# Optimization experiments

Measured on AMD Instinct MI355X. Metric: run time of the kernel, lower is better.

Reference implementation:

```python
import jax, jax.numpy as jnp
import numpy as np

IN_C, HID, L, NN, BS, OUT = 32, 128, 4, 64, 512, 3
N = NN * BS  # total graph vertices
EPS_LN = 1e-5
EPS_SM = 1e-16  # PyG softmax eps


def setup_inputs() -> dict:
    key = jax.random.key(0)
    ks = jax.random.split(key, 16)
    E = 524288
    x = jax.random.normal(ks[0], (N, IN_C), dtype=jnp.float32)
    edge_index = jax.random.randint(ks[1], (2, E), 0, N, dtype=jnp.int64)
    s = 0.1
    # first GAT layer (in -> hidden)
    W0 = jax.random.normal(ks[2], (IN_C, HID), dtype=jnp.float32) * s
    att_src0 = jax.random.normal(ks[3], (HID,), dtype=jnp.float32) * s
    att_dst0 = jax.random.normal(ks[4], (HID,), dtype=jnp.float32) * s
    bias0 = jnp.zeros((HID,), dtype=jnp.float32)
    # residual GAT layers (hidden -> hidden), stacked over L
    W_res = jax.random.normal(ks[5], (L, HID, HID), dtype=jnp.float32) * s
    att_src_res = jax.random.normal(ks[6], (L, HID), dtype=jnp.float32) * s
    att_dst_res = jax.random.normal(ks[7], (L, HID), dtype=jnp.float32) * s
    bias_res = jnp.zeros((L, HID), dtype=jnp.float32)
    gamma = jnp.ones((L, HID), dtype=jnp.float32)
    beta = jnp.zeros((L, HID), dtype=jnp.float32)
    # per-node predictor heads
    W1p = jax.random.normal(ks[8], (NN, HID, HID // 2), dtype=jnp.float32) * s
    W2p = jax.random.normal(ks[9], (NN, HID // 2, OUT), dtype=jnp.float32) * s
    return {"x": x, "edge_index": edge_index, "W0": W0, "att_src0": att_src0,
            "att_dst0": att_dst0, "bias0": bias0, "W_res": W_res,
            "att_src_res": att_src_res, "att_dst_res": att_dst_res,
            "bias_res": bias_res, "gamma": gamma, "beta": beta,
            "W1p": W1p, "W2p": W2p}


def _gat(x, src, dst, W, a_src, a_dst, b):
    # PyG GATConv, heads=1, negative_slope=0.2, self-loops already appended
    h = x @ W                                   # [N, H]
    a_s = (h * a_src).sum(-1)                   # [N]
    a_d = (h * a_dst).sum(-1)                   # [N]
    e = jax.nn.leaky_relu(a_s[src] + a_d[dst], 0.2)   # [E]
    m = jax.ops.segment_max(e, dst, num_segments=N)
    e = jnp.exp(e - m[dst])
    z = jax.ops.segment_sum(e, dst, num_segments=N)
    alpha = e / (z[dst] + EPS_SM)               # [E]
    out = jax.ops.segment_sum(h[src] * alpha[:, None], dst, num_segments=N)
    return out + b


def _layernorm(x, g, b):
    mu = x.mean(-1, keepdims=True)
    var = ((x - mu) ** 2).mean(-1, keepdims=True)
    return (x - mu) * jax.lax.rsqrt(var + EPS_LN) * g + b


def reference(x, edge_index, W0, att_src0, att_dst0, bias0, W_res,
              att_src_res, att_dst_res, bias_res, gamma, beta, W1p, W2p):
    loops = jnp.arange(N, dtype=edge_index.dtype)
    src = jnp.concatenate([edge_index[0], loops])
    dst = jnp.concatenate([edge_index[1], loops])
    # first GAT + relu
    h = jax.nn.relu(_gat(x, src, dst, W0, att_src0, att_dst0, bias0))
    # res+ blocks: h = h + conv(dropout(act(norm(h))))  (dropout=identity, eval)
    for i in range(L):
        t = jax.nn.relu(_layernorm(h, gamma[i], beta[i]))
        t = _gat(t, src, dst, W_res[i], att_src_res[i], att_dst_res[i], bias_res[i])
        h = h + t
    h = jax.nn.relu(_layernorm(h, gamma[0], beta[0]))
    # per-node predictor heads
    h = h.reshape(NN, BS, HID)
    t = jax.nn.relu(jnp.einsum('nbh,nhk->nbk', h, W1p))
    logits = jnp.einsum('nbk,nko->nbo', t, W2p)
    return jax.nn.softmax(logits, axis=-1)   # softmax over class dim (dim=1 per node slice)
```

## Files before the change

### kernel.cpp

```cpp
#include <hip/hip_runtime.h>
#include <hip/hip_fp8.h>
#include <math.h>

#define NND   32768
#define HIDD  128
#define NHEAD 64
#define BSS   512
#define OUTC  3
#define NTILES (NND / 16)
#define CSLOT 80

typedef _Float16 half_t;
typedef __attribute__((ext_vector_type(8))) _Float16 half8;
typedef __attribute__((ext_vector_type(4))) float f32x4;

__device__ __forceinline__ unsigned enc_fp8x4(float a, float b, float c, float d) {
    __hip_fp8x4_e4m3 q(make_float4(a, b, c, d));
    return (unsigned)q.__x;
}
__device__ __forceinline__ float4 dec_fp8x4(unsigned v) {
    __hip_fp8x4_e4m3 t; t.__x = (__hip_fp8x4_storage_t)v;
    return (float4)t;
}

// ... 43 lines not shown
                int tt = task - 64; int l = 1 + tt / 256; int r = tt % 256;
                int k = r >> 1; sd = r & 1;
                row = W_res + (size_t)(l - 1) * 16384 + k * 128;
                att = (sd ? ad_res : as_res) + (l - 1) * 128;
                slot = l * 128 + k;
            }
            float s = 0.f;
            for (int n = 0; n < 128; ++n) s += row[n] * att[n];
            (sd ? wvec + 640 : wvec)[slot] = s;
        }
    } else if (b < 1090) {
        int b2 = b - 578;
        const float* xs = x + (size_t)b2 * 64 * 32;
        half_t* xd = xh + (size_t)b2 * 64 * 32;
        for (int i = tid; i < 1024; i += 256) {
            float2 v = ((const float2*)xs)[i];
            union { unsigned u; half_t h[2]; } cv;
            cv.h[0] = (half_t)v.x; cv.h[1] = (half_t)v.y;
            ((unsigned*)xd)[i] = cv.u;
        }
    } else {
        int j = (b - 1090) * 256 + tid;
        int Etot = E + NND;
        if (j >= Etot) return;
        int src, dst;
        if (j < E) { src = ei[j]; dst = ei[E + j]; }
        else       { src = j - E; dst = j - E; }
        int rank = atomicAdd(&counts[dst], 1);
        if (rank < CSLOT) csrd[(size_t)dst * CSLOT + rank] = src;
    }
}

__global__ __launch_bounds__(256) void a0_kernel(const half_t* __restrict__ xh,
        const float* __restrict__ wvec,
        float* __restrict__ a_s, float* __restrict__ a_d) {
    int tid = threadIdx.x;
    __shared__ float ws0[32], wd0[32];
    if (tid < 32) { ws0[tid] = wvec[tid]; wd0[tid] = wvec[640 + tid]; }
    __syncthreads();
    int g = blockIdx.x * 256 + tid;
    int node = g >> 2, part = g & 3;
    half8 xv = *(const half8*)&xh[(size_t)node * 32 + part * 8];
    float s = 0.f, d2 = 0.f;
#pragma unroll
    for (int j = 0; j < 8; ++j) { float f = (float)xv[j]; s += f * ws0[part * 8 + j]; d2 += f * wd0[part * 8 + j]; }
    s += __shfl_xor(s, 1); s += __shfl_xor(s, 2);
    d2 += __shfl_xor(d2, 1); d2 += __shfl_xor(d2, 2);
    if (part == 0) { a_s[node] = s; a_d[node] = d2; }
}


struct MArgs {
    const half_t* xh;
    const int* csrd;
    const int* counts;
    const half_t* W0t;
    const half_t* Wh;
    const float* bias0;
    const float* b_res;
    const float* gamma;
    const float* beta;
    const float* wvec;
    float* a_s0; float* a_d0; float* a_s1; float* a_d1;
    unsigned char* Th8a; unsigned char* Th8b;
    half_t* Hh;
    const half_t* W1h;
    const float* W2p;
    float* out;
};

struct SmemT {
    half_t Pt[16][136];
    union U {
        float vv[16][132];
        struct { int s[1024]; float p[1024]; } sp;
    } u;
    int cntl[16];
    float adv[16];
};

__device__ __forceinline__ void stage_sp(const float* __restrict__ a_sv,
        const int* __restrict__ csrd, int n0, int base, int tid, SmemT& sm) {
#pragma unroll
    for (int it = 0; it < 4; ++it) {
        int i = it * 256 + tid;
        int ln = i >> 6, k = i & 63;
        int sN = 0; float pN = 0.f;
        if (base + k < sm.cntl[ln]) {
            sN = csrd[(size_t)(n0 + ln) * CSLOT + base + k];
            float tt = a_sv[sN] + sm.adv[ln];
            tt = (tt > 0.f) ? tt : 0.2f * tt;
            pN = __expf(tt);
        }
        sm.u.sp.s[i] = sN;
        sm.u.sp.p[i] = pN;
    }
}

__device__ __forceinline__ void agg_node_f8(const unsigned char* __restrict__ F8,
        const SmemT& sm, int ln, int base, int lane, int q, int r15,
        float acc[8], float& pzv) {
    int rem = sm.cntl[ln] - base;
    if (rem <= 0) return;
    int cnt = rem > 64 ? 64 : rem;
    pzv += sm.u.sp.p[ln * 64 + lane];
    const int* sl = &sm.u.sp.s[ln * 64];
    const float* pl = &sm.u.sp.p[ln * 64];
    for (int k4 = 0; k4 < cnt; k4 += 16) {
        int s0 = sl[k4 + q],       s1 = sl[k4 + 4 + q];
        int s2 = sl[k4 + 8 + q],   s3 = sl[k4 + 12 + q];
        float p0 = pl[k4 + q],     p1 = pl[k4 + 4 + q];
        float p2 = pl[k4 + 8 + q], p3 = pl[k4 + 12 + q];
        uint2 r0 = *(const uint2*)&F8[(size_t)s0 * HIDD + r15 * 8];
        uint2 r1 = *(const uint2*)&F8[(size_t)s1 * HIDD + r15 * 8];
        uint2 r2 = *(const uint2*)&F8[(size_t)s2 * HIDD + r15 * 8];
        uint2 r3 = *(const uint2*)&F8[(size_t)s3 * HIDD + r15 * 8];
        float4 f;
        f = dec_fp8x4(r0.x); acc[0]+=p0*f.x; acc[1]+=p0*f.y; acc[2]+=p0*f.z; acc[3]+=p0*f.w;
        f = dec_fp8x4(r0.y); acc[4]+=p0*f.x; acc[5]+=p0*f.y; acc[6]+=p0*f.z; acc[7]+=p0*f.w;
        f = dec_fp8x4(r1.x); acc[0]+=p1*f.x; acc[1]+=p1*f.y; acc[2]+=p1*f.z; acc[3]+=p1*f.w;
        f = dec_fp8x4(r1.y); acc[4]+=p1*f.x; acc[5]+=p1*f.y; acc[6]+=p1*f.z; acc[7]+=p1*f.w;
        f = dec_fp8x4(r2.x); acc[0]+=p2*f.x; acc[1]+=p2*f.y; acc[2]+=p2*f.z; acc[3]+=p2*f.w;
        f = dec_fp8x4(r2.y); acc[4]+=p2*f.x; acc[5]+=p2*f.y; acc[6]+=p2*f.z; acc[7]+=p2*f.w;
        f = dec_fp8x4(r3.x); acc[0]+=p3*f.x; acc[1]+=p3*f.y; acc[2]+=p3*f.z; acc[3]+=p3*f.w;
        f = dec_fp8x4(r3.y); acc[4]+=p3*f.x; acc[5]+=p3*f.y; acc[6]+=p3*f.z; acc[7]+=p3*f.w;
    }
}

__device__ __forceinline__ void finish_res(SmemT& sm, int wv, int pass, int q, int r15,
        float acc[2][8], float pz2[2]) {
#pragma unroll
    for (int ln2 = 0; ln2 < 2; ++ln2) {
        int ln = wv * 4 + pass * 2 + ln2;
        float z = pz2[ln2];
#pragma unroll
        for (int o = 32; o; o >>= 1) z += __shfl_xor(z, o);
#pragma unroll
        for (int i = 0; i < 8; ++i) {
            acc[ln2][i] += __shfl_xor(acc[ln2][i], 16);
            acc[ln2][i] += __shfl_xor(acc[ln2][i], 32);
        }
        if (q == 0) {
            float inv = 1.f / (z + 1e-16f);
            union { int4 v; half_t hh[8]; } u;
#pragma unroll
            for (int i = 0; i < 8; ++i) u.hh[i] = (half_t)(acc[ln2][i] * inv);
            *(int4*)&sm.Pt[ln][r15 * 8] = u.v;
        }
    }
}

__device__ __forceinline__ void agg2_res(const unsigned char* __restrict__ F8,
        const float* __restrict__ a_sv, const float* __restrict__ a_dv,
        const int* __restrict__ csrd, const int* __restrict__ counts,
        int n0, int tid, int wv, int lane, int q, int r15, SmemT& sm) {
    if (tid < 16) { sm.cntl[tid] = counts[n0 + tid]; sm.adv[tid] = a_dv[n0 + tid]; }
    __syncthreads();
    int maxd = 0;
    for (int i = 0; i < 16; ++i) { int d = sm.cntl[i]; maxd = d > maxd ? d : maxd; }
    if (maxd <= 64) {
        stage_sp(a_sv, csrd, n0, 0, tid, sm);
        __syncthreads();
#pragma unroll
        for (int pass = 0; pass < 2; ++pass) {
            float acc[2][8];
            float pz2[2] = {0.f, 0.f};
#pragma unroll
            for (int a = 0; a < 2; ++a)
#pragma unroll
                for (int i = 0; i < 8; ++i) acc[a][i] = 0.f;
#pragma unroll
            for (int ln2 = 0; ln2 < 2; ++ln2)
                agg_node_f8(F8, sm, wv * 4 + pass * 2 + ln2, 0, lane, q, r15, acc[ln2], pz2[ln2]);
            finish_res(sm, wv, pass, q, r15, acc, pz2);
        }
    } else {
#pragma unroll
        for (int pass = 0; pass < 2; ++pass) {
            float acc[2][8];
            float pz2[2] = {0.f, 0.f};
#pragma unroll
            for (int a = 0; a < 2; ++a)
#pragma unroll
                for (int i = 0; i < 8; ++i) acc[a][i] = 0.f;
            for (int base = 0; base < maxd; base += 64) {
                __syncthreads();
                stage_sp(a_sv, csrd, n0, base, tid, sm);
                __syncthreads();
#pragma unroll
                for (int ln2 = 0; ln2 < 2; ++ln2)
                    agg_node_f8(F8, sm, wv * 4 + pass * 2 + ln2, base, lane, q, r15, acc[ln2], pz2[ln2]);
            }
            finish_res(sm, wv, pass, q, r15, acc, pz2);
        }
    }
}

__device__ __forceinline__ void agg2_l0(const half_t* __restrict__ xh,
        const float* __restrict__ a_sv, const float* __restrict__ a_dv,
        const int* __restrict__ csrd, const int* __restrict__ counts,
        int n0, int tid, int wv, int lane, int q, int r15, SmemT& sm) {
    if (tid < 16) { sm.cntl[tid] = counts[n0 + tid]; sm.adv[tid] = a_dv[n0 + tid]; }
    __syncthreads();
    int maxd = 0;
    for (int i = 0; i < 16; ++i) { int d = sm.cntl[i]; maxd = d > maxd ? d : maxd; }
    float acc[4][2];
    float pz[4];
#pragma unroll
    for (int a = 0; a < 4; ++a) { pz[a] = 0.f; acc[a][0] = 0.f; acc[a][1] = 0.f; }
    for (int base = 0; base < maxd; base += 64) {
        __syncthreads();
        stage_sp(a_sv, csrd, n0, base, tid, sm);
        __syncthreads();
#pragma unroll
        for (int ln4 = 0; ln4 < 4; ++ln4) {
            int ln = wv * 4 + ln4;
            int rem = sm.cntl[ln] - base;
            if (rem <= 0) continue;
            int cnt = rem > 64 ? 64 : rem;
            pz[ln4] += sm.u.sp.p[ln * 64 + lane];
            const int* sl = &sm.u.sp.s[ln * 64];
            const float* pl = &sm.u.sp.p[ln * 64];
            for (int k4 = 0; k4 < cnt; k4 += 16) {
                int s0 = sl[k4 + q],      s1 = sl[k4 + 4 + q];
                int s2 = sl[k4 + 8 + q],  s3 = sl[k4 + 12 + q];
                float p0 = pl[k4 + q],    p1 = pl[k4 + 4 + q];
                float p2 = pl[k4 + 8 + q], p3 = pl[k4 + 12 + q];
                union { unsigned u; half_t h[2]; } u0, u1, u2, u3;
                u0.u = *(const unsigned*)&xh[(size_t)s0 * 32 + r15 * 2];
                u1.u = *(const unsigned*)&xh[(size_t)s1 * 32 + r15 * 2];
                u2.u = *(const unsigned*)&xh[(size_t)s2 * 32 + r15 * 2];
                u3.u = *(const unsigned*)&xh[(size_t)s3 * 32 + r15 * 2];
                acc[ln4][0] += p0 * (float)u0.h[0] + p1 * (float)u1.h[0] + p2 * (float)u2.h[0] + p3 * (float)u3.h[0];
                acc[ln4][1] += p0 * (float)u0.h[1] + p1 * (float)u1.h[1] + p2 * (float)u2.h[1] + p3 * (float)u3.h[1];
            }
        }
    }
#pragma unroll
    for (int ln4 = 0; ln4 < 4; ++ln4) {
        int ln = wv * 4 + ln4;
        float z = pz[ln4];
#pragma unroll
        for (int o = 32; o; o >>= 1) z += __shfl_xor(z, o);
#pragma unroll
        for (int i = 0; i < 2; ++i) {
            acc[ln4][i] += __shfl_xor(acc[ln4][i], 16);
            acc[ln4][i] += __shfl_xor(acc[ln4][i], 32);
        }
        if (q == 0) {
            float inv = 1.f / (z + 1e-16f);
            union { unsigned u; half_t h[2]; } w2;
            w2.h[0] = (half_t)(acc[ln4][0] * inv);
            w2.h[1] = (half_t)(acc[ln4][1] * inv);
            *(unsigned*)&sm.Pt[ln][r15 * 2] = w2.u;
        }
    }
}

template <int K, bool RES>
__device__ __forceinline__ void gemm_epi_tile(int n0, int tid, int wv, int q, int r15,
        const half_t* __restrict__ Whl, const float* __restrict__ bias,
        half_t* __restrict__ Hh, unsigned char* __restrict__ Th8o,
        const float* __restrict__ gamma, const float* __restrict__ beta,
        const float* __restrict__ wsn, const float* __restrict__ wdn,
        float* __restrict__ as_out, float* __restrict__ ad_out,
        half_t Pt[16][136], float vv[16][132]) {
    half8 afrag[K / 32];
#pragma unroll
    for (int s = 0; s < K / 32; ++s)
        afrag[s] = *(const half8*)&Pt[r15][s * 32 + q * 8];
    f32x4 acc2[2];
#pragma unroll
    for (int i = 0; i < 2; ++i) {
        int ct = wv * 2 + i;
        f32x4 c = {0.f, 0.f, 0.f, 0.f};
#pragma unroll
        for (int s = 0; s < K / 32; ++s) {
            half8 bfrag = *(const half8*)&Whl[(size_t)(ct * 16 + r15) * K + s * 32 + q * 8];
            c = __builtin_amdgcn_mfma_f32_16x16x32_f16(afrag[s], bfrag, c, 0, 0, 0);
        }
        acc2[i] = c;
    }
#pragma unroll
    for (int i = 0; i < 2; ++i)
#pragma unroll
        for (int r = 0; r < 4; ++r)
            vv[q * 4 + r][wv * 32 + i * 16 + r15] = acc2[i][r];
    __syncthreads();
    int grp = tid >> 4, sub = tid & 15;
    int node = n0 + grp;
    const float* vrow = &vv[grp][sub * 8];
    float v8[8];
    {
        float4 bi0 = *(const float4*)&bias[sub * 8];
        float4 bi1 = *(const float4*)&bias[sub * 8 + 4];
        v8[0] = vrow[0] + bi0.x; v8[1] = vrow[1] + bi0.y;
        v8[2] = vrow[2] + bi0.z; v8[3] = vrow[3] + bi0.w;
        v8[4] = vrow[4] + bi1.x; v8[5] = vrow[5] + bi1.y;
        v8[6] = vrow[6] + bi1.z; v8[7] = vrow[7] + bi1.w;
    }
    if (RES) {
        half8 hold = *(const half8*)&Hh[(size_t)node * HIDD + sub * 8];
#pragma unroll
        for (int j = 0; j < 8; ++j) v8[j] += (float)hold[j];
    } else {
#pragma unroll
        for (int j = 0; j < 8; ++j) v8[j] = fmaxf(v8[j], 0.f);
    }
    union { int4 i4; half_t h[8]; } hw;
#pragma unroll
    for (int j = 0; j < 8; ++j) hw.h[j] = (half_t)v8[j];
    *(int4*)&Hh[(size_t)node * HIDD + sub * 8] = hw.i4;
    float sum = 0.f;
#pragma unroll
    for (int j = 0; j < 8; ++j) sum += v8[j];
#pragma unroll
    for (int o = 8; o; o >>= 1) sum += __shfl_xor(sum, o);
    float mu = sum * (1.f / HIDD);
    float var = 0.f;
#pragma unroll
    for (int j = 0; j < 8; ++j) { float dx = v8[j] - mu; var += dx * dx; }
#pragma unroll
    for (int o = 8; o; o >>= 1) var += __shfl_xor(var, o);
    float rs = rsqrtf(var * (1.f / HIDD) + 1e-5f);
    float asn, adn;
    uint2 tw;
    {
        float4 g4 = *(const float4*)&gamma[sub * 8];
        float4 b4 = *(const float4*)&beta[sub * 8];
        float t0 = fmaxf((v8[0] - mu) * rs * g4.x + b4.x, 0.f);
        float t1 = fmaxf((v8[1] - mu) * rs * g4.y + b4.y, 0.f);
        float t2 = fmaxf((v8[2] - mu) * rs * g4.z + b4.z, 0.f);
        float t3 = fmaxf((v8[3] - mu) * rs * g4.w + b4.w, 0.f);
        float4 w4 = *(const float4*)&wsn[sub * 8];
        float4 d4 = *(const float4*)&wdn[sub * 8];
        asn = t0 * w4.x; asn += t1 * w4.y; asn += t2 * w4.z; asn += t3 * w4.w;
        adn = t0 * d4.x; adn += t1 * d4.y; adn += t2 * d4.z; adn += t3 * d4.w;
        tw.x = enc_fp8x4(t0, t1, t2, t3);
    }
    {
        float4 g4 = *(const float4*)&gamma[sub * 8 + 4];
        float4 b4 = *(const float4*)&beta[sub * 8 + 4];
        float t4 = fmaxf((v8[4] - mu) * rs * g4.x + b4.x, 0.f);
        float t5 = fmaxf((v8[5] - mu) * rs * g4.y + b4.y, 0.f);
        float t6 = fmaxf((v8[6] - mu) * rs * g4.z + b4.z, 0.f);
        float t7 = fmaxf((v8[7] - mu) * rs * g4.w + b4.w, 0.f);
        float4 w4 = *(const float4*)&wsn[sub * 8 + 4];
        float4 d4 = *(const float4*)&wdn[sub * 8 + 4];
        asn += t4 * w4.x; asn += t5 * w4.y; asn += t6 * w4.z; asn += t7 * w4.w;
        adn += t4 * d4.x; adn += t5 * d4.y; adn += t6 * d4.z; adn += t7 * d4.w;
        tw.y = enc_fp8x4(t4, t5, t6, t7);
    }
    *(uint2*)&Th8o[(size_t)node * HIDD + sub * 8] = tw;
#pragma unroll
    for (int o = 8; o; o >>= 1) { asn += __shfl_xor(asn, o); adn += __shfl_xor(adn, o); }
    if (sub == 0) { as_out[node] = asn; ad_out[node] = adn; }
}

__device__ __forceinline__ void last_tile(int n0, int tid, int wv, int q, int r15,
        const MArgs& A, half_t Pt[16][136], float vv[16][132]) {
    const half_t* Whl = A.Wh + (size_t)3 * 16384;
    half8 afrag[4];
#pragma unroll
    for (int s = 0; s < 4; ++s)
        afrag[s] = *(const half8*)&Pt[r15][s * 32 + q * 8];
    f32x4 acc2[2];
#pragma unroll
    for (int i = 0; i < 2; ++i) {
        int ct = wv * 2 + i;
        f32x4 c = {0.f, 0.f, 0.f, 0.f};
#pragma unroll
        for (int s = 0; s < 4; ++s) {
            half8 bfrag = *(const half8*)&Whl[(size_t)(ct * 16 + r15) * 128 + s * 32 + q * 8];
            c = __builtin_amdgcn_mfma_f32_16x16x32_f16(afrag[s], bfrag, c, 0, 0, 0);
        }
        acc2[i] = c;
    }
#pragma unroll
    for (int i = 0; i < 2; ++i)
#pragma unroll
        for (int r = 0; r < 4; ++r)
            vv[q * 4 + r][wv * 32 + i * 16 + r15] = acc2[i][r];
    __syncthreads();
    int grp = tid >> 4, sub = tid & 15;
    const float* bias = A.b_res + 3 * HIDD;
    float4 bi0 = *(const float4*)&bias[sub * 8],    bi1 = *(const float4*)&bias[sub * 8 + 4];
    float4 g0  = *(const float4*)&A.gamma[sub * 8], g1  = *(const float4*)&A.gamma[sub * 8 + 4];
    float4 be0 = *(const float4*)&A.beta[sub * 8],  be1 = *(const float4*)&A.beta[sub * 8 + 4];
    float bi[8] = {bi0.x,bi0.y,bi0.z,bi0.w,bi1.x,bi1.y,bi1.z,bi1.w};
    float gg[8] = {g0.x,g0.y,g0.z,g0.w,g1.x,g1.y,g1.z,g1.w};
    float be[8] = {be0.x,be0.y,be0.z,be0.w,be1.x,be1.y,be1.z,be1.w};
    int node = n0 + grp;
    float v8[8];
    half8 hold = *(const half8*)&A.Hh[(size_t)node * HIDD + sub * 8];
#pragma unroll
    for (int j = 0; j < 8; ++j) v8[j] = vv[grp][sub * 8 + j] + bi[j] + (float)hold[j];
    float sum = 0.f;
#pragma unroll
    for (int j = 0; j < 8; ++j) sum += v8[j];
#pragma unroll
    for (int o = 8; o; o >>= 1) sum += __shfl_xor(sum, o);
    float mu = sum * (1.f / HIDD);
    float var = 0.f;
#pragma unroll
    for (int j = 0; j < 8; ++j) { float dx = v8[j] - mu; var += dx * dx; }
#pragma unroll
    for (int o = 8; o; o >>= 1) var += __shfl_xor(var, o);
    float rs = rsqrtf(var * (1.f / HIDD) + 1e-5f);
    union { int4 i4; half_t h[8]; } u;
#pragma unroll
    for (int j = 0; j < 8; ++j)
        u.h[j] = (half_t)fmaxf((v8[j] - mu) * rs * gg[j] + be[j], 0.f);
    __syncthreads();
    *(int4*)&Pt[grp][sub * 8] = u.i4;
    __syncthreads();
    int head = n0 >> 9;
    const half_t* W1g = A.W1h + (size_t)head * 64 * 128;
    half8 pa[4];
#pragma unroll
    for (int s = 0; s < 4; ++s)
        pa[s] = *(const half8*)&Pt[r15][s * 32 + q * 8];
    int n2 = wv * 16 + r15;
    f32x4 c = {0.f, 0.f, 0.f, 0.f};
#pragma unroll
    for (int s = 0; s < 4; ++s) {
        half8 bfrag = *(const half8*)&W1g[(size_t)n2 * 128 + s * 32 + q * 8];
        c = __builtin_amdgcn_mfma_f32_16x16x32_f16(pa[s], bfrag, c, 0, 0, 0);
    }
    float w2a = A.W2p[(size_t)head * 192 + n2 * 3 + 0];
    float w2b = A.W2p[(size_t)head * 192 + n2 * 3 + 1];
    float w2c = A.W2p[(size_t)head * 192 + n2 * 3 + 2];
    float lg[3][4];
#pragma unroll
    for (int r = 0; r < 4; ++r) {
        float t = fmaxf(c[r], 0.f);
        lg[0][r] = t * w2a;
        lg[1][r] = t * w2b;
        lg[2][r] = t * w2c;
    }
#pragma unroll
    for (int o = 8; o; o >>= 1)
#pragma unroll
        for (int oo = 0; oo < 3; ++oo)
#pragma unroll
            for (int r = 0; r < 4; ++r) lg[oo][r] += __shfl_xor(lg[oo][r], o);
    __syncthreads();
    if (r15 == 0) {
#pragma unroll
        for (int r = 0; r < 4; ++r)
#pragma unroll
            for (int oo = 0; oo < 3; ++oo) vv[q * 4 + r][wv * 3 + oo] = lg[oo][r];
    }
    __syncthreads();
    if (tid < 16) {
        float l0 = vv[tid][0] + vv[tid][3] + vv[tid][6] + vv[tid][9];
        float l1 = vv[tid][1] + vv[tid][4] + vv[tid][7] + vv[tid][10];
        float l2 = vv[tid][2] + vv[tid][5] + vv[tid][8] + vv[tid][11];
        float mx = fmaxf(l0, fmaxf(l1, l2));
        float e0 = __expf(l0 - mx), e1 = __expf(l1 - mx), e2 = __expf(l2 - mx);
        float inv = 1.f / (e0 + e1 + e2);
        float* op = A.out + (size_t)(n0 + tid) * OUTC;
        op[0] = e0 * inv; op[1] = e1 * inv; op[2] = e2 * inv;
    }
}

__global__ __launch_bounds__(256, 8) void fused6_l0(MArgs A) {
    __shared__ SmemT sm;
    int tid = threadIdx.x;
    int wv = tid >> 6, lane = tid & 63;
    int q = lane >> 4, r15 = lane & 15;
    int n0 = blockIdx.x * 16;
    agg2_l0(A.xh, A.a_s0, A.a_d0, A.csrd, A.counts, n0, tid, wv, lane, q, r15, sm);
    __syncthreads();
    gemm_epi_tile<32, false>(n0, tid, wv, q, r15, A.W0t, A.bias0, A.Hh, A.Th8a,
        A.gamma, A.beta, A.wvec + 128, A.wvec + 640 + 128, A.a_s1, A.a_d1, sm.Pt, sm.u.vv);
}

template <int L>
__global__ __launch_bounds__(256, 8) void fused6_res(MArgs A) {
    __shared__ SmemT sm;
    int tid = threadIdx.x;
    int wv = tid >> 6, lane = tid & 63;
    int q = lane >> 4, r15 = lane & 15;
    int n0 = blockIdx.x * 16;
    const unsigned char* Ts = (L & 1) ? A.Th8b : A.Th8a;
    unsigned char* Td       = (L & 1) ? A.Th8a : A.Th8b;
    const float* asv = (L & 1) ? A.a_s0 : A.a_s1;
    const float* adv = (L & 1) ? A.a_d0 : A.a_d1;
    float* aso = (L & 1) ? A.a_s1 : A.a_s0;
    float* ado = (L & 1) ? A.a_d1 : A.a_d0;
    agg2_res(Ts, asv, adv, A.csrd, A.counts, n0, tid, wv, lane, q, r15, sm);
    __syncthreads();
    gemm_epi_tile<128, true>(n0, tid, wv, q, r15, A.Wh + (size_t)L * 16384,
        A.b_res + L * HIDD, A.Hh, Td, A.gamma + (L + 1) * HIDD, A.beta + (L + 1) * HIDD,
        A.wvec + (L + 2) * 128, A.wvec + 640 + (L + 2) * 128, aso, ado, sm.Pt, sm.u.vv);
}

__global__ __launch_bounds__(256, 4) void fused6_last(MArgs A) {
    __shared__ SmemT sm;
    int tid = threadIdx.x;
    int wv = tid >> 6, lane = tid & 63;
    int q = lane >> 4, r15 = lane & 15;
    int n0 = blockIdx.x * 16;
    agg2_res(A.Th8b, A.a_s0, A.a_d0, A.csrd, A.counts, n0, tid, wv, lane, q, r15, sm);
    __syncthreads();
    last_tile(n0, tid, wv, q, r15, A, sm.Pt, sm.u.vv);
}

extern "C" void kernel_launch(void* const* d_in, const int* in_sizes, int n_in,
                              void* d_out, int out_size, void* d_ws, size_t ws_size,
                              hipStream_t stream) {
    const float* x        = (const float*)d_in[0];
    const int*   ei       = (const int*)d_in[1];
    const float* W0       = (const float*)d_in[2];
    const float* att_src0 = (const float*)d_in[3];
    const float* att_dst0 = (const float*)d_in[4];
    const float* bias0    = (const float*)d_in[5];
    const float* W_res    = (const float*)d_in[6];
    const float* as_res   = (const float*)d_in[7];
    const float* ad_res   = (const float*)d_in[8];
    const float* b_res    = (const float*)d_in[9];
    const float* gamma    = (const float*)d_in[10];
    const float* beta     = (const float*)d_in[11];
    const float* W1p      = (const float*)d_in[12];
    const float* W2p      = (const float*)d_in[13];
    float* out = (float*)d_out;

    int E = in_sizes[1] / 2;
    int Etot = E + NND;

    char* p = (char*)d_ws;
    auto alloc = [&](size_t bytes) { void* r = (void*)p; p += (bytes + 255) & ~(size_t)255; return r; };
    int*    counts  = (int*)alloc((size_t)NND * 4);
    int*    csrd    = (int*)alloc((size_t)NND * CSLOT * 4);
    half_t* xh      = (half_t*)alloc((size_t)NND * 32 * 2);
    unsigned char* Th8a = (unsigned char*)alloc((size_t)NND * HIDD);
    unsigned char* Th8b = (unsigned char*)alloc((size_t)NND * HIDD);
    half_t* Hh      = (half_t*)alloc((size_t)NND * HIDD * 2);
    float*  a_s0    = (float*)alloc((size_t)NND * 4);
    float*  a_d0    = (float*)alloc((size_t)NND * 4);
    float*  a_s1    = (float*)alloc((size_t)NND * 4);
    float*  a_d1    = (float*)alloc((size_t)NND * 4);
    half_t* Wh      = (half_t*)alloc((size_t)4 * HIDD * HIDD * 2);
    half_t* W1h     = (half_t*)alloc((size_t)NHEAD * 64 * HIDD * 2);
    half_t* W0t     = (half_t*)alloc((size_t)HIDD * 32 * 2);
    float*  wvec    = (float*)alloc((size_t)1280 * 4);

    int egrid = (Etot + 255) / 256;

    hipMemsetAsync(counts, 0, (size_t)NND * 4, stream);
    prep_kernel<<<1090 + egrid, 256, 0, stream>>>(W0, W_res, W1p, att_src0, att_dst0,
        as_res, ad_res, x, ei, E, Wh, W1h, W0t, wvec, xh, counts, csrd);
    a0_kernel<<<512, 256, 0, stream>>>(xh, wvec, a_s0, a_d0);

    MArgs ma;
    ma.xh = xh; ma.csrd = csrd; ma.counts = counts;
    ma.W0t = W0t; ma.Wh = Wh;
    ma.bias0 = bias0; ma.b_res = b_res;
    ma.gamma = gamma; ma.beta = beta; ma.wvec = wvec;
    ma.a_s0 = a_s0; ma.a_d0 = a_d0; ma.a_s1 = a_s1; ma.a_d1 = a_d1;
    ma.Th8a = Th8a; ma.Th8b = Th8b; ma.Hh = Hh;
    ma.W1h = W1h; ma.W2p = W2p; ma.out = out;

    fused6_l0<<<NTILES, 256, 0, stream>>>(ma);
    fused6_res<0><<<NTILES, 256, 0, stream>>>(ma);
    fused6_res<1><<<NTILES, 256, 0, stream>>>(ma);
    fused6_res<2><<<NTILES, 256, 0, stream>>>(ma);
    fused6_last<<<NTILES, 256, 0, stream>>>(ma);
}
```

Before: 292.7 us.

## Double block size to 512 threads so each wave aggregates two nodes

```diff
diff --git a/kernel.cpp b/kernel.cpp
--- a/kernel.cpp
+++ b/kernel.cpp
@@ -149,8 +149,8 @@
 __device__ __forceinline__ void stage_sp(const float* __restrict__ a_sv,
         const int* __restrict__ csrd, int n0, int base, int tid, SmemT& sm) {
 #pragma unroll
-    for (int it = 0; it < 4; ++it) {
-        int i = it * 256 + tid;
+    for (int it = 0; it < 2; ++it) {
+        int i = it * 512 + tid;
         int ln = i >> 6, k = i & 63;
         int sN = 0; float pN = 0.f;
         if (base + k < sm.cntl[ln]) {
@@ -164,59 +164,6 @@
     }
 }
 
-__device__ __forceinline__ void agg_node_f8(const unsigned char* __restrict__ F8,
-        const SmemT& sm, int ln, int base, int lane, int q, int r15,
-        float acc[8], float& pzv) {
-    int rem = sm.cntl[ln] - base;
-    if (rem <= 0) return;
-    int cnt = rem > 64 ? 64 : rem;
-    pzv += sm.u.sp.p[ln * 64 + lane];
-    const int* sl = &sm.u.sp.s[ln * 64];
-    const float* pl = &sm.u.sp.p[ln * 64];
-    for (int k4 = 0; k4 < cnt; k4 += 16) {
-        int s0 = sl[k4 + q],       s1 = sl[k4 + 4 + q];
-        int s2 = sl[k4 + 8 + q],   s3 = sl[k4 + 12 + q];
-        float p0 = pl[k4 + q],     p1 = pl[k4 + 4 + q];
-        float p2 = pl[k4 + 8 + q], p3 = pl[k4 + 12 + q];
-        uint2 r0 = *(const uint2*)&F8[(size_t)s0 * HIDD + r15 * 8];
-        uint2 r1 = *(const uint2*)&F8[(size_t)s1 * HIDD + r15 * 8];
-        uint2 r2 = *(const uint2*)&F8[(size_t)s2 * HIDD + r15 * 8];
-        uint2 r3 = *(const uint2*)&F8[(size_t)s3 * HIDD + r15 * 8];
-        float4 f;
-        f = dec_fp8x4(r0.x); acc[0]+=p0*f.x; acc[1]+=p0*f.y; acc[2]+=p0*f.z; acc[3]+=p0*f.w;
-        f = dec_fp8x4(r0.y); acc[4]+=p0*f.x; acc[5]+=p0*f.y; acc[6]+=p0*f.z; acc[7]+=p0*f.w;
-        f = dec_fp8x4(r1.x); acc[0]+=p1*f.x; acc[1]+=p1*f.y; acc[2]+=p1*f.z; acc[3]+=p1*f.w;
-        f = dec_fp8x4(r1.y); acc[4]+=p1*f.x; acc[5]+=p1*f.y; acc[6]+=p1*f.z; acc[7]+=p1*f.w;
-        f = dec_fp8x4(r2.x); acc[0]+=p2*f.x; acc[1]+=p2*f.y; acc[2]+=p2*f.z; acc[3]+=p2*f.w;
-        f = dec_fp8x4(r2.y); acc[4]+=p2*f.x; acc[5]+=p2*f.y; acc[6]+=p2*f.z; acc[7]+=p2*f.w;
-        f = dec_fp8x4(r3.x); acc[0]+=p3*f.x; acc[1]+=p3*f.y; acc[2]+=p3*f.z; acc[3]+=p3*f.w;
-        f = dec_fp8x4(r3.y); acc[4]+=p3*f.x; acc[5]+=p3*f.y; acc[6]+=p3*f.z; acc[7]+=p3*f.w;
-    }
-}
-
-__device__ __forceinline__ void finish_res(SmemT& sm, int wv, int pass, int q, int r15,
-        float acc[2][8], float pz2[2]) {
-#pragma unroll
-    for (int ln2 = 0; ln2 < 2; ++ln2) {
-        int ln = wv * 4 + pass * 2 + ln2;
-        float z = pz2[ln2];
-#pragma unroll
-        for (int o = 32; o; o >>= 1) z += __shfl_xor(z, o);
-#pragma unroll
-        for (int i = 0; i < 8; ++i) {
-            acc[ln2][i] += __shfl_xor(acc[ln2][i], 16);
-            acc[ln2][i] += __shfl_xor(acc[ln2][i], 32);
-        }
-        if (q == 0) {
-            float inv = 1.f / (z + 1e-16f);
-            union { int4 v; half_t hh[8]; } u;
-#pragma unroll
-            for (int i = 0; i < 8; ++i) u.hh[i] = (half_t)(acc[ln2][i] * inv);
-            *(int4*)&sm.Pt[ln][r15 * 8] = u.v;
-        }
-    }
-}
-
 __device__ __forceinline__ void agg2_res(const unsigned char* __restrict__ F8,
         const float* __restrict__ a_sv, const float* __restrict__ a_dv,
         const int* __restrict__ csrd, const int* __restrict__ counts,
@@ -225,40 +172,74 @@
     __syncthreads();
     int maxd = 0;
     for (int i = 0; i < 16; ++i) { int d = sm.cntl[i]; maxd = d > maxd ? d : maxd; }
-    if (maxd <= 64) {
-        stage_sp(a_sv, csrd, n0, 0, tid, sm);
+    float acc[2][8];
+    float pz[2];
+#pragma unroll
+    for (int a = 0; a < 2; ++a) {
+        pz[a] = 0.f;
+#pragma unroll
+        for (int i = 0; i < 8; ++i) acc[a][i] = 0.f;
+    }
+    for (int base = 0; base < maxd; base += 64) {
         __syncthreads();
-#pragma unroll
-        for (int pass = 0; pass < 2; ++pass) {
-            float acc[2][8];
-            float pz2[2] = {0.f, 0.f};
-#pragma unroll
-            for (int a = 0; a < 2; ++a)
-#pragma unroll
-                for (int i = 0; i < 8; ++i) acc[a][i] = 0.f;
-#pragma unroll
-            for (int ln2 = 0; ln2 < 2; ++ln2)
-                agg_node_f8(F8, sm, wv * 4 + pass * 2 + ln2, 0, lane, q, r15, acc[ln2], pz2[ln2]);
-            finish_res(sm, wv, pass, q, r15, acc, pz2);
-        }
-    } else {
-#pragma unroll
-        for (int pass = 0; pass < 2; ++pass) {
-            float acc[2][8];
-            float pz2[2] = {0.f, 0.f};
-#pragma unroll
-            for (int a = 0; a < 2; ++a)
-#pragma unroll
-                for (int i = 0; i < 8; ++i) acc[a][i] = 0.f;
-            for (int base = 0; base < maxd; base += 64) {
-                __syncthreads();
-                stage_sp(a_sv, csrd, n0, base, tid, sm);
-                __syncthreads();
-#pragma unroll
-                for (int ln2 = 0; ln2 < 2; ++ln2)
-                    agg_node_f8(F8, sm, wv * 4 + pass * 2 + ln2, base, lane, q, r15, acc[ln2], pz2[ln2]);
+        stage_sp(a_sv, csrd, n0, base, tid, sm);
+        __syncthreads();
+#pragma unroll
+        for (int ln2 = 0; ln2 < 2; ++ln2) {
+            int ln = wv * 2 + ln2;
+            int rem = sm.cntl[ln] - base;
+            if (rem <= 0) continue;
+            int cnt = rem > 64 ? 64 : rem;
+            pz[ln2] += sm.u.sp.p[ln * 64 + lane];
+            const int* sl = &sm.u.sp.s[ln * 64];
+            const float* pl = &sm.u.sp.p[ln * 64];
+            int full = cnt & ~15;
+            int k4 = 0;
+            for (; k4 < full; k4 += 16) {
+                int s0 = sl[k4 + q],      s1 = sl[k4 + 4 + q];
+                int s2 = sl[k4 + 8 + q],  s3 = sl[k4 + 12 + q];
+                float p0 = pl[k4 + q],    p1 = pl[k4 + 4 + q];
+                float p2 = pl[k4 + 8 + q], p3 = pl[k4 + 12 + q];
+                uint2 r0 = *(const uint2*)&F8[(size_t)s0 * HIDD + r15 * 8];
+                uint2 r1 = *(const uint2*)&F8[(size_t)s1 * HIDD + r15 * 8];
+                uint2 r2 = *(const uint2*)&F8[(size_t)s2 * HIDD + r15 * 8];
+                uint2 r3 = *(const uint2*)&F8[(size_t)s3 * HIDD + r15 * 8];
+                float4 f;
+                f = dec_fp8x4(r0.x); acc[ln2][0]+=p0*f.x; acc[ln2][1]+=p0*f.y; acc[ln2][2]+=p0*f.z; acc[ln2][3]+=p0*f.w;
+                f = dec_fp8x4(r0.y); acc[ln2][4]+=p0*f.x; acc[ln2][5]+=p0*f.y; acc[ln2][6]+=p0*f.z; acc[ln2][7]+=p0*f.w;
+                f = dec_fp8x4(r1.x); acc[ln2][0]+=p1*f.x; acc[ln2][1]+=p1*f.y; acc[ln2][2]+=p1*f.z; acc[ln2][3]+=p1*f.w;
+                f = dec_fp8x4(r1.y); acc[ln2][4]+=p1*f.x; acc[ln2][5]+=p1*f.y; acc[ln2][6]+=p1*f.z; acc[ln2][7]+=p1*f.w;
+                f = dec_fp8x4(r2.x); acc[ln2][0]+=p2*f.x; acc[ln2][1]+=p2*f.y; acc[ln2][2]+=p2*f.z; acc[ln2][3]+=p2*f.w;
+                f = dec_fp8x4(r2.y); acc[ln2][4]+=p2*f.x; acc[ln2][5]+=p2*f.y; acc[ln2][6]+=p2*f.z; acc[ln2][7]+=p2*f.w;
+                f = dec_fp8x4(r3.x); acc[ln2][0]+=p3*f.x; acc[ln2][1]+=p3*f.y; acc[ln2][2]+=p3*f.z; acc[ln2][3]+=p3*f.w;
+                f = dec_fp8x4(r3.y); acc[ln2][4]+=p3*f.x; acc[ln2][5]+=p3*f.y; acc[ln2][6]+=p3*f.z; acc[ln2][7]+=p3*f.w;
             }
-            finish_res(sm, wv, pass, q, r15, acc, pz2);
+            for (; k4 < cnt; k4 += 4) {
+                int s0 = sl[k4 + q]; float p0 = pl[k4 + q];
+                uint2 r0 = *(const uint2*)&F8[(size_t)s0 * HIDD + r15 * 8];
+                float4 f;
+                f = dec_fp8x4(r0.x); acc[ln2][0]+=p0*f.x; acc[ln2][1]+=p0*f.y; acc[ln2][2]+=p0*f.z; acc[ln2][3]+=p0*f.w;
+                f = dec_fp8x4(r0.y); acc[ln2][4]+=p0*f.x; acc[ln2][5]+=p0*f.y; acc[ln2][6]+=p0*f.z; acc[ln2][7]+=p0*f.w;
+            }
+        }
+    }
+#pragma unroll
+    for (int ln2 = 0; ln2 < 2; ++ln2) {
+        int ln = wv * 2 + ln2;
+        float z = pz[ln2];
+#pragma unroll
+        for (int o = 32; o; o >>= 1) z += __shfl_xor(z, o);
+#pragma unroll
+        for (int i = 0; i < 8; ++i) {
+            acc[ln2][i] += __shfl_xor(acc[ln2][i], 16);
+            acc[ln2][i] += __shfl_xor(acc[ln2][i], 32);
+        }
+        if (q == 0) {
+            float inv = 1.f / (z + 1e-16f);
+            union { int4 v; half_t hh[8]; } u;
+#pragma unroll
+            for (int i = 0; i < 8; ++i) u.hh[i] = (half_t)(acc[ln2][i] * inv);
+            *(int4*)&sm.Pt[ln][r15 * 8] = u.v;
         }
     }
 }
@@ -271,24 +252,26 @@
     __syncthreads();
     int maxd = 0;
     for (int i = 0; i < 16; ++i) { int d = sm.cntl[i]; maxd = d > maxd ? d : maxd; }
-    float acc[4][2];
-    float pz[4];
-#pragma unroll
-    for (int a = 0; a < 4; ++a) { pz[a] = 0.f; acc[a][0] = 0.f; acc[a][1] = 0.f; }
+    float acc[2][2];
+    float pz[2];
+#pragma unroll
+    for (int a = 0; a < 2; ++a) { pz[a] = 0.f; acc[a][0] = 0.f; acc[a][1] = 0.f; }
     for (int base = 0; base < maxd; base += 64) {
         __syncthreads();
         stage_sp(a_sv, csrd, n0, base, tid, sm);
         __syncthreads();
 #pragma unroll
-        for (int ln4 = 0; ln4 < 4; ++ln4) {
-            int ln = wv * 4 + ln4;
+        for (int ln2 = 0; ln2 < 2; ++ln2) {
+            int ln = wv * 2 + ln2;
             int rem = sm.cntl[ln] - base;
             if (rem <= 0) continue;
             int cnt = rem > 64 ? 64 : rem;
-            pz[ln4] += sm.u.sp.p[ln * 64 + lane];
+            pz[ln2] += sm.u.sp.p[ln * 64 + lane];
             const int* sl = &sm.u.sp.s[ln * 64];
             const float* pl = &sm.u.sp.p[ln * 64];
-            for (int k4 = 0; k4 < cnt; k4 += 16) {
+            int full = cnt & ~15;
+            int k4 = 0;
+            for (; k4 < full; k4 += 16) {
                 int s0 = sl[k4 + q],      s1 = sl[k4 + 4 + q];
                 int s2 = sl[k4 + 8 + q],  s3 = sl[k4 + 12 + q];
                 float p0 = pl[k4 + q],    p1 = pl[k4 + 4 + q];
@@ -298,27 +281,34 @@
                 u1.u = *(const unsigned*)&xh[(size_t)s1 * 32 + r15 * 2];
                 u2.u = *(const unsigned*)&xh[(size_t)s2 * 32 + r15 * 2];
                 u3.u = *(const unsigned*)&xh[(size_t)s3 * 32 + r15 * 2];
-                acc[ln4][0] += p0 * (float)u0.h[0] + p1 * (float)u1.h[0] + p2 * (float)u2.h[0] + p3 * (float)u3.h[0];
-                acc[ln4][1] += p0 * (float)u0.h[1] + p1 * (float)u1.h[1] + p2 * (float)u2.h[1] + p3 * (float)u3.h[1];
+                acc[ln2][0] += p0 * (float)u0.h[0] + p1 * (float)u1.h[0] + p2 * (float)u2.h[0] + p3 * (float)u3.h[0];
+                acc[ln2][1] += p0 * (float)u0.h[1] + p1 * (float)u1.h[1] + p2 * (float)u2.h[1] + p3 * (float)u3.h[1];
             }
-        }
-    }
-#pragma unroll
-    for (int ln4 = 0; ln4 < 4; ++ln4) {
-        int ln = wv * 4 + ln4;
-        float z = pz[ln4];
+            for (; k4 < cnt; k4 += 4) {
+                int s0 = sl[k4 + q]; float p0 = pl[k4 + q];
+                union { unsigned u; half_t h[2]; } u0;
+                u0.u = *(const unsigned*)&xh[(size_t)s0 * 32 + r15 * 2];
+                acc[ln2][0] += p0 * (float)u0.h[0];
+                acc[ln2][1] += p0 * (float)u0.h[1];
+            }
+        }
+    }
+#pragma unroll
+    for (int ln2 = 0; ln2 < 2; ++ln2) {
+        int ln = wv * 2 + ln2;
+        float z = pz[ln2];
 #pragma unroll
         for (int o = 32; o; o >>= 1) z += __shfl_xor(z, o);
 #pragma unroll
         for (int i = 0; i < 2; ++i) {
-            acc[ln4][i] += __shfl_xor(acc[ln4][i], 16);
-            acc[ln4][i] += __shfl_xor(acc[ln4][i], 32);
+            acc[ln2][i] += __shfl_xor(acc[ln2][i], 16);
+            acc[ln2][i] += __shfl_xor(acc[ln2][i], 32);
         }
         if (q == 0) {
             float inv = 1.f / (z + 1e-16f);
             union { unsigned u; half_t h[2]; } w2;
-            w2.h[0] = (half_t)(acc[ln4][0] * inv);
-            w2.h[1] = (half_t)(acc[ln4][1] * inv);
+            w2.h[0] = (half_t)(acc[ln2][0] * inv);
+            w2.h[1] = (half_t)(acc[ln2][1] * inv);
             *(unsigned*)&sm.Pt[ln][r15 * 2] = w2.u;
         }
     }
@@ -336,92 +326,88 @@
 #pragma unroll
     for (int s = 0; s < K / 32; ++s)
         afrag[s] = *(const half8*)&Pt[r15][s * 32 + q * 8];
-    f32x4 acc2[2];
-#pragma unroll
-    for (int i = 0; i < 2; ++i) {
-        int ct = wv * 2 + i;
+    {
         f32x4 c = {0.f, 0.f, 0.f, 0.f};
 #pragma unroll
         for (int s = 0; s < K / 32; ++s) {
-            half8 bfrag = *(const half8*)&Whl[(size_t)(ct * 16 + r15) * K + s * 32 + q * 8];
+            half8 bfrag = *(const half8*)&Whl[(size_t)(wv * 16 + r15) * K + s * 32 + q * 8];
             c = __builtin_amdgcn_mfma_f32_16x16x32_f16(afrag[s], bfrag, c, 0, 0, 0);
         }
-        acc2[i] = c;
-    }
-#pragma unroll
-    for (int i = 0; i < 2; ++i)
 #pragma unroll
         for (int r = 0; r < 4; ++r)
-            vv[q * 4 + r][wv * 32 + i * 16 + r15] = acc2[i][r];
-    __syncthreads();
-    int grp = tid >> 4, sub = tid & 15;
-    int node = n0 + grp;
-    const float* vrow = &vv[grp][sub * 8];
-    float v8[8];
-    {
-        float4 bi0 = *(const float4*)&bias[sub * 8];
-        float4 bi1 = *(const float4*)&bias[sub * 8 + 4];
-        v8[0] = vrow[0] + bi0.x; v8[1] = vrow[1] + bi0.y;
-        v8[2] = vrow[2] + bi0.z; v8[3] = vrow[3] + bi0.w;
-        v8[4] = vrow[4] + bi1.x; v8[5] = vrow[5] + bi1.y;
-        v8[6] = vrow[6] + bi1.z; v8[7] = vrow[7] + bi1.w;
-    }
-    if (RES) {
-        half8 hold = *(const half8*)&Hh[(size_t)node * HIDD + sub * 8];
-#pragma unroll
-        for (int j = 0; j < 8; ++j) v8[j] += (float)hold[j];
-    } else {
-#pragma unroll
-        for (int j = 0; j < 8; ++j) v8[j] = fmaxf(v8[j], 0.f);
-    }
-    union { int4 i4; half_t h[8]; } hw;
-#pragma unroll
-    for (int j = 0; j < 8; ++j) hw.h[j] = (half_t)v8[j];
-    *(int4*)&Hh[(size_t)node * HIDD + sub * 8] = hw.i4;
-    float sum = 0.f;
-#pragma unroll
-    for (int j = 0; j < 8; ++j) sum += v8[j];
-#pragma unroll
-    for (int o = 8; o; o >>= 1) sum += __shfl_xor(sum, o);
-    float mu = sum * (1.f / HIDD);
-    float var = 0.f;
-#pragma unroll
-    for (int j = 0; j < 8; ++j) { float dx = v8[j] - mu; var += dx * dx; }
-#pragma unroll
-    for (int o = 8; o; o >>= 1) var += __shfl_xor(var, o);
-    float rs = rsqrtf(var * (1.f / HIDD) + 1e-5f);
-    float asn, adn;
-    uint2 tw;
-    {
-        float4 g4 = *(const float4*)&gamma[sub * 8];
-        float4 b4 = *(const float4*)&beta[sub * 8];
-        float t0 = fmaxf((v8[0] - mu) * rs * g4.x + b4.x, 0.f);
-        float t1 = fmaxf((v8[1] - mu) * rs * g4.y + b4.y, 0.f);
-        float t2 = fmaxf((v8[2] - mu) * rs * g4.z + b4.z, 0.f);
-        float t3 = fmaxf((v8[3] - mu) * rs * g4.w + b4.w, 0.f);
-        float4 w4 = *(const float4*)&wsn[sub * 8];
-        float4 d4 = *(const float4*)&wdn[sub * 8];
-        asn = t0 * w4.x; asn += t1 * w4.y; asn += t2 * w4.z; asn += t3 * w4.w;
-        adn = t0 * d4.x; adn += t1 * d4.y; adn += t2 * d4.z; adn += t3 * d4.w;
-        tw.x = enc_fp8x4(t0, t1, t2, t3);
-    }
-    {
-        float4 g4 = *(const float4*)&gamma[sub * 8 + 4];
-        float4 b4 = *(const float4*)&beta[sub * 8 + 4];
-        float t4 = fmaxf((v8[4] - mu) * rs * g4.x + b4.x, 0.f);
-        float t5 = fmaxf((v8[5] - mu) * rs * g4.y + b4.y, 0.f);
-        float t6 = fmaxf((v8[6] - mu) * rs * g4.z + b4.z, 0.f);
-        float t7 = fmaxf((v8[7] - mu) * rs * g4.w + b4.w, 0.f);
-        float4 w4 = *(const float4*)&wsn[sub * 8 + 4];
-        float4 d4 = *(const float4*)&wdn[sub * 8 + 4];
-        asn += t4 * w4.x; asn += t5 * w4.y; asn += t6 * w4.z; asn += t7 * w4.w;
-        adn += t4 * d4.x; adn += t5 * d4.y; adn += t6 * d4.z; adn += t7 * d4.w;
-        tw.y = enc_fp8x4(t4, t5, t6, t7);
-    }
-    *(uint2*)&Th8o[(size_t)node * HIDD + sub * 8] = tw;
-#pragma unroll
-    for (int o = 8; o; o >>= 1) { asn += __shfl_xor(asn, o); adn += __shfl_xor(adn, o); }
-    if (sub == 0) { as_out[node] = asn; ad_out[node] = adn; }
+            vv[q * 4 + r][wv * 16 + r15] = c[r];
+    }
+    __syncthreads();
+    if (tid < 256) {
+        int grp = tid >> 4, sub = tid & 15;
+        int node = n0 + grp;
+        const float* vrow = &vv[grp][sub * 8];
+        float v8[8];
+        {
+            float4 bi0 = *(const float4*)&bias[sub * 8];
+            float4 bi1 = *(const float4*)&bias[sub * 8 + 4];
+            v8[0] = vrow[0] + bi0.x; v8[1] = vrow[1] + bi0.y;
+            v8[2] = vrow[2] + bi0.z; v8[3] = vrow[3] + bi0.w;
+            v8[4] = vrow[4] + bi1.x; v8[5] = vrow[5] + bi1.y;
+            v8[6] = vrow[6] + bi1.z; v8[7] = vrow[7] + bi1.w;
+        }
+        if (RES) {
+            half8 hold = *(const half8*)&Hh[(size_t)node * HIDD + sub * 8];
+#pragma unroll
+            for (int j = 0; j < 8; ++j) v8[j] += (float)hold[j];
+        } else {
+#pragma unroll
+            for (int j = 0; j < 8; ++j) v8[j] = fmaxf(v8[j], 0.f);
+        }
+        union { int4 i4; half_t h[8]; } hw;
+#pragma unroll
+        for (int j = 0; j < 8; ++j) hw.h[j] = (half_t)v8[j];
+        *(int4*)&Hh[(size_t)node * HIDD + sub * 8] = hw.i4;
+        float sum = 0.f;
+#pragma unroll
+        for (int j = 0; j < 8; ++j) sum += v8[j];
+#pragma unroll
+        for (int o = 8; o; o >>= 1) sum += __shfl_xor(sum, o);
+        float mu = sum * (1.f / HIDD);
+        float var = 0.f;
+#pragma unroll
+        for (int j = 0; j < 8; ++j) { float dx = v8[j] - mu; var += dx * dx; }
+#pragma unroll
+        for (int o = 8; o; o >>= 1) var += __shfl_xor(var, o);
+        float rs = rsqrtf(var * (1.f / HIDD) + 1e-5f);
+        float asn, adn;
+        uint2 tw;
+        {
+            float4 g4 = *(const float4*)&gamma[sub * 8];
+            float4 b4 = *(const float4*)&beta[sub * 8];
+            float t0 = fmaxf((v8[0] - mu) * rs * g4.x + b4.x, 0.f);
+            float t1 = fmaxf((v8[1] - mu) * rs * g4.y + b4.y, 0.f);
+            float t2 = fmaxf((v8[2] - mu) * rs * g4.z + b4.z, 0.f);
+            float t3 = fmaxf((v8[3] - mu) * rs * g4.w + b4.w, 0.f);
+            float4 w4 = *(const float4*)&wsn[sub * 8];
+            float4 d4 = *(const float4*)&wdn[sub * 8];
+            asn = t0 * w4.x; asn += t1 * w4.y; asn += t2 * w4.z; asn += t3 * w4.w;
+            adn = t0 * d4.x; adn += t1 * d4.y; adn += t2 * d4.z; adn += t3 * d4.w;
+            tw.x = enc_fp8x4(t0, t1, t2, t3);
+        }
+        {
+            float4 g4 = *(const float4*)&gamma[sub * 8 + 4];
+            float4 b4 = *(const float4*)&beta[sub * 8 + 4];
+            float t4 = fmaxf((v8[4] - mu) * rs * g4.x + b4.x, 0.f);
+            float t5 = fmaxf((v8[5] - mu) * rs * g4.y + b4.y, 0.f);
+            float t6 = fmaxf((v8[6] - mu) * rs * g4.z + b4.z, 0.f);
+            float t7 = fmaxf((v8[7] - mu) * rs * g4.w + b4.w, 0.f);
+            float4 w4 = *(const float4*)&wsn[sub * 8 + 4];
+            float4 d4 = *(const float4*)&wdn[sub * 8 + 4];
+            asn += t4 * w4.x; asn += t5 * w4.y; asn += t6 * w4.z; asn += t7 * w4.w;
+            adn += t4 * d4.x; adn += t5 * d4.y; adn += t6 * d4.z; adn += t7 * d4.w;
+            tw.y = enc_fp8x4(t4, t5, t6, t7);
+        }
+        *(uint2*)&Th8o[(size_t)node * HIDD + sub * 8] = tw;
+#pragma unroll
+        for (int o = 8; o; o >>= 1) { asn += __shfl_xor(asn, o); adn += __shfl_xor(adn, o); }
+        if (sub == 0) { as_out[node] = asn; ad_out[node] = adn; }
+    }
 }
 
 __device__ __forceinline__ void last_tile(int n0, int tid, int wv, int q, int r15,
@@ -431,88 +417,86 @@
 #pragma unroll
     for (int s = 0; s < 4; ++s)
         afrag[s] = *(const half8*)&Pt[r15][s * 32 + q * 8];
-    f32x4 acc2[2];
-#pragma unroll
-    for (int i = 0; i < 2; ++i) {
-        int ct = wv * 2 + i;
+    {
         f32x4 c = {0.f, 0.f, 0.f, 0.f};
 #pragma unroll
         for (int s = 0; s < 4; ++s) {
-            half8 bfrag = *(const half8*)&Whl[(size_t)(ct * 16 + r15) * 128 + s * 32 + q * 8];
+            half8 bfrag = *(const half8*)&Whl[(size_t)(wv * 16 + r15) * 128 + s * 32 + q * 8];
             c = __builtin_amdgcn_mfma_f32_16x16x32_f16(afrag[s], bfrag, c, 0, 0, 0);
         }
-        acc2[i] = c;
-    }
-#pragma unroll
-    for (int i = 0; i < 2; ++i)
 #pragma unroll
         for (int r = 0; r < 4; ++r)
-            vv[q * 4 + r][wv * 32 + i * 16 + r15] = acc2[i][r];
-    __syncthreads();
+            vv[q * 4 + r][wv * 16 + r15] = c[r];
+    }
+    __syncthreads();
+    union { int4 i4; half_t h[8]; } u;
     int grp = tid >> 4, sub = tid & 15;
-    const float* bias = A.b_res + 3 * HIDD;
-    float4 bi0 = *(const float4*)&bias[sub * 8],    bi1 = *(const float4*)&bias[sub * 8 + 4];
-    float4 g0  = *(const float4*)&A.gamma[sub * 8], g1  = *(const float4*)&A.gamma[sub * 8 + 4];
-    float4 be0 = *(const float4*)&A.beta[sub * 8],  be1 = *(const float4*)&A.beta[sub * 8 + 4];
-    float bi[8] = {bi0.x,bi0.y,bi0.z,bi0.w,bi1.x,bi1.y,bi1.z,bi1.w};
-    float gg[8] = {g0.x,g0.y,g0.z,g0.w,g1.x,g1.y,g1.z,g1.w};
-    float be[8] = {be0.x,be0.y,be0.z,be0.w,be1.x,be1.y,be1.z,be1.w};
-    int node = n0 + grp;
-    float v8[8];
-    half8 hold = *(const half8*)&A.Hh[(size_t)node * HIDD + sub * 8];
-#pragma unroll
-    for (int j = 0; j < 8; ++j) v8[j] = vv[grp][sub * 8 + j] + bi[j] + (float)hold[j];
-    float sum = 0.f;
-#pragma unroll
-    for (int j = 0; j < 8; ++j) sum += v8[j];
-#pragma unroll
-    for (int o = 8; o; o >>= 1) sum += __shfl_xor(sum, o);
-    float mu = sum * (1.f / HIDD);
-    float var = 0.f;
-#pragma unroll
-    for (int j = 0; j < 8; ++j) { float dx = v8[j] - mu; var += dx * dx; }
-#pragma unroll
-    for (int o = 8; o; o >>= 1) var += __shfl_xor(var, o);
-    float rs = rsqrtf(var * (1.f / HIDD) + 1e-5f);
-    union { int4 i4; half_t h[8]; } u;
-#pragma unroll
-    for (int j = 0; j < 8; ++j)
-        u.h[j] = (half_t)fmaxf((v8[j] - mu) * rs * gg[j] + be[j], 0.f);
-    __syncthreads();
-    *(int4*)&Pt[grp][sub * 8] = u.i4;
+    if (tid < 256) {
+        const float* bias = A.b_res + 3 * HIDD;
+        float4 bi0 = *(const float4*)&bias[sub * 8],    bi1 = *(const float4*)&bias[sub * 8 + 4];
+        float4 g0  = *(const float4*)&A.gamma[sub * 8], g1  = *(const float4*)&A.gamma[sub * 8 + 4];
+        float4 be0 = *(const float4*)&A.beta[sub * 8],  be1 = *(const float4*)&A.beta[sub * 8 + 4];
+        float bi[8] = {bi0.x,bi0.y,bi0.z,bi0.w,bi1.x,bi1.y,bi1.z,bi1.w};
+        float gg[8] = {g0.x,g0.y,g0.z,g0.w,g1.x,g1.y,g1.z,g1.w};
+        float be[8] = {be0.x,be0.y,be0.z,be0.w,be1.x,be1.y,be1.z,be1.w};
+        int node = n0 + grp;
+        float v8[8];
+        half8 hold = *(const half8*)&A.Hh[(size_t)node * HIDD + sub * 8];
+#pragma unroll
+        for (int j = 0; j < 8; ++j) v8[j] = vv[grp][sub * 8 + j] + bi[j] + (float)hold[j];
+        float sum = 0.f;
+#pragma unroll
+        for (int j = 0; j < 8; ++j) sum += v8[j];
+#pragma unroll
+        for (int o = 8; o; o >>= 1) sum += __shfl_xor(sum, o);
+        float mu = sum * (1.f / HIDD);
+        float var = 0.f;
+#pragma unroll
+        for (int j = 0; j < 8; ++j) { float dx = v8[j] - mu; var += dx * dx; }
+#pragma unroll
+        for (int o = 8; o; o >>= 1) var += __shfl_xor(var, o);
+        float rs = rsqrtf(var * (1.f / HIDD) + 1e-5f);
+#pragma unroll
+        for (int j = 0; j < 8; ++j)
+            u.h[j] = (half_t)fmaxf((v8[j] - mu) * rs * gg[j] + be[j], 0.f);
+    }
+    __syncthreads();
+    if (tid < 256) *(int4*)&Pt[grp][sub * 8] = u.i4;
     __syncthreads();
     int head = n0 >> 9;
-    const half_t* W1g = A.W1h + (size_t)head * 64 * 128;
-    half8 pa[4];
-#pragma unroll
-    for (int s = 0; s < 4; ++s)
-        pa[s] = *(const half8*)&Pt[r15][s * 32 + q * 8];
-    int n2 = wv * 16 + r15;
-    f32x4 c = {0.f, 0.f, 0.f, 0.f};
-#pragma unroll
-    for (int s = 0; s < 4; ++s) {
-        half8 bfrag = *(const half8*)&W1g[(size_t)n2 * 128 + s * 32 + q * 8];
-        c = __builtin_amdgcn_mfma_f32_16x16x32_f16(pa[s], bfrag, c, 0, 0, 0);
-    }
-    float w2a = A.W2p[(size_t)head * 192 + n2 * 3 + 0];
-    float w2b = A.W2p[(size_t)head * 192 + n2 * 3 + 1];
-    float w2c = A.W2p[(size_t)head * 192 + n2 * 3 + 2];
     float lg[3][4];
-#pragma unroll
-    for (int r = 0; r < 4; ++r) {
-        float t = fmaxf(c[r], 0.f);
-        lg[0][r] = t * w2a;
-        lg[1][r] = t * w2b;
-        lg[2][r] = t * w2c;
-    }
-#pragma unroll
-    for (int o = 8; o; o >>= 1)
-#pragma unroll
-        for (int oo = 0; oo < 3; ++oo)
-#pragma unroll
-            for (int r = 0; r < 4; ++r) lg[oo][r] += __shfl_xor(lg[oo][r], o);
-    __syncthreads();
-    if (r15 == 0) {
+    if (wv < 4) {
+        const half_t* W1g = A.W1h + (size_t)head * 64 * 128;
+        half8 pa[4];
+#pragma unroll
+        for (int s = 0; s < 4; ++s)
+            pa[s] = *(const half8*)&Pt[r15][s * 32 + q * 8];
+        int n2 = wv * 16 + r15;
+        f32x4 c = {0.f, 0.f, 0.f, 0.f};
+#pragma unroll
+        for (int s = 0; s < 4; ++s) {
+            half8 bfrag = *(const half8*)&W1g[(size_t)n2 * 128 + s * 32 + q * 8];
+            c = __builtin_amdgcn_mfma_f32_16x16x32_f16(pa[s], bfrag, c, 0, 0, 0);
+        }
+        float w2a = A.W2p[(size_t)head * 192 + n2 * 3 + 0];
+        float w2b = A.W2p[(size_t)head * 192 + n2 * 3 + 1];
+        float w2c = A.W2p[(size_t)head * 192 + n2 * 3 + 2];
+#pragma unroll
+        for (int r = 0; r < 4; ++r) {
+            float t = fmaxf(c[r], 0.f);
+            lg[0][r] = t * w2a;
+            lg[1][r] = t * w2b;
+            lg[2][r] = t * w2c;
+        }
+#pragma unroll
+        for (int o = 8; o; o >>= 1)
+#pragma unroll
+            for (int oo = 0; oo < 3; ++oo)
+#pragma unroll
+                for (int r = 0; r < 4; ++r) lg[oo][r] += __shfl_xor(lg[oo][r], o);
+    }
+    __syncthreads();
+    if (wv < 4 && r15 == 0) {
 #pragma unroll
         for (int r = 0; r < 4; ++r)
 #pragma unroll
@@ -531,7 +515,7 @@
     }
 }
 
-__global__ __launch_bounds__(256, 8) void fused6_l0(MArgs A) {
+__global__ __launch_bounds__(512, 8) void fused7_l0(MArgs A) {
     __shared__ SmemT sm;
     int tid = threadIdx.x;
     int wv = tid >> 6, lane = tid & 63;
@@ -544,7 +528,7 @@
 }
 
 template <int L>
-__global__ __launch_bounds__(256, 8) void fused6_res(MArgs A) {
+__global__ __launch_bounds__(512, 8) void fused7_res(MArgs A) {
     __shared__ SmemT sm;
     int tid = threadIdx.x;
     int wv = tid >> 6, lane = tid & 63;
@@ -563,7 +547,7 @@
         A.wvec + (L + 2) * 128, A.wvec + 640 + (L + 2) * 128, aso, ado, sm.Pt, sm.u.vv);
 }
 
-__global__ __launch_bounds__(256, 4) void fused6_last(MArgs A) {
+__global__ __launch_bounds__(512, 4) void fused7_last(MArgs A) {
     __shared__ SmemT sm;
     int tid = threadIdx.x;
     int wv = tid >> 6, lane = tid & 63;
@@ -629,9 +613,9 @@
     ma.Th8a = Th8a; ma.Th8b = Th8b; ma.Hh = Hh;
     ma.W1h = W1h; ma.W2p = W2p; ma.out = out;
 
-    fused6_l0<<<NTILES, 256, 0, stream>>>(ma);
-    fused6_res<0><<<NTILES, 256, 0, stream>>>(ma);
-    fused6_res<1><<<NTILES, 256, 0, stream>>>(ma);
-    fused6_res<2><<<NTILES, 256, 0, stream>>>(ma);
-    fused6_last<<<NTILES, 256, 0, stream>>>(ma);
-}
+    fused7_l0<<<NTILES, 512, 0, stream>>>(ma);
+    fused7_res<0><<<NTILES, 512, 0, stream>>>(ma);
+    fused7_res<1><<<NTILES, 512, 0, stream>>>(ma);
+    fused7_res<2><<<NTILES, 512, 0, stream>>>(ma);
+    fused7_last<<<NTILES, 512, 0, stream>>>(ma);
+}
```

Measured after the change: 330.2 us. 12.8% more time.
